# Kernel tuning notes

Hardware: AMD Instinct MI355X
Metric: run time of the kernel (lower is better)

Reference implementation:

```python
import jax, jax.numpy as jnp
import numpy as np

B, S, R = 1, 128, 384          # batch, n_seq (MSA rows), n_res
C_M, C_Z, H, D = 256, 128, 8, 32  # msa channels, pair channels, heads, head dim


def layernorm(x, g, b, eps=1e-5):
    mu = jnp.mean(x, axis=-1, keepdims=True)
    var = jnp.var(x, axis=-1, keepdims=True)
    return (x - mu) * jax.lax.rsqrt(var + eps) * g + b


def setup_inputs() -> dict:
    key = jax.random.key(0)
    ks = jax.random.split(key, 10)
    w = lambda k, shape: jax.random.normal(k, shape, jnp.float32) * 0.02
    return {
        "msa_act": jax.random.normal(ks[0], (B, S, R, C_M), jnp.float32),
        "pair_act": jax.random.normal(ks[1], (B, R, R, C_Z), jnp.float32),
        "msa_mask": jnp.ones((B, S, R), jnp.float32),
        "qn_g": jnp.ones((C_M,), jnp.float32),
        "qn_b": jnp.zeros((C_M,), jnp.float32),
        "pn_g": jnp.ones((C_Z,), jnp.float32),
        "pn_b": jnp.zeros((C_Z,), jnp.float32),
        "w_pair": w(ks[2], (C_Z, H)),           # feat_2d_weights (no bias)
        "wq": w(ks[3], (C_M, H, D)),
        "wk": w(ks[4], (C_M, H, D)),
        "wv": w(ks[5], (C_M, H, D)),
        "wg": w(ks[6], (C_M, H, D)),            # gating linear
        "bg": jnp.ones((H, D), jnp.float32),     # gating bias (AF2 inits to 1)
        "wo": w(ks[7], (H, D, C_M)),             # output projection
        "bo": jnp.zeros((C_M,), jnp.float32),
    }


def reference(msa_act, pair_act, msa_mask, qn_g, qn_b, pn_g, pn_b,
              w_pair, wq, wk, wv, wg, bg, wo, bo):
    # pair bias: LN + Linear(c_z -> H), -> [B, 1, H, R, R]
    z = jnp.einsum('bijc,ch->bhij', layernorm(pair_act, pn_g, pn_b), w_pair)[:, None]
    # mask bias: [B, S, 1, 1, R]
    mask_bias = (1e9 * (msa_mask - 1.0))[:, :, None, None, :]

    m = layernorm(msa_act, qn_g, qn_b)
    q = jnp.einsum('bsrc,chd->bshrd', m, wq) * (D ** -0.5)
    k = jnp.einsum('bsrc,chd->bshrd', m, wk)
    v = jnp.einsum('bsrc,chd->bshrd', m, wv)

    logits = jnp.einsum('bshqd,bshkd->bshqk', q, k) + mask_bias + z  # [B,S,H,R,R]
    a = jax.nn.softmax(logits, axis=-1)
    o = jnp.einsum('bshqk,bshkd->bsqhd', a, v)                       # [B,S,R,H,D]

    g = jax.nn.sigmoid(jnp.einsum('bsrc,chd->bsrhd', m, wg) + bg)
    out = jnp.einsum('bsrhd,hdc->bsrc', o * g, wo) + bo              # [B,S,R,C_M]
    return out
```

## Files before the change

kernel.cpp:

```cpp
#include <hip/hip_runtime.h>
#include <hip/hip_bf16.h>

typedef unsigned int uint;
typedef unsigned short ushortT;
typedef __attribute__((ext_vector_type(8))) short bf16x8;
typedef __attribute__((ext_vector_type(4))) float f32x4;

#define S_ 128
#define R_ 384
#define CM 256
#define CZ 128
#define H_ 8
#define D_ 32
#define SR (S_*R_)
#define RRTOT (R_*R_)
#define SHRD (S_*H_*R_*D_)

__device__ __forceinline__ float bf2f(ushortT u) {
    return __uint_as_float(((uint)u) << 16);
}
__device__ __forceinline__ ushortT f2bf(float f) {
    uint x = __float_as_uint(f);
    x += 0x7FFFu + ((x >> 16) & 1u);
    return (ushortT)(x >> 16);
}
__device__ __forceinline__ uint pack_bf2(float lo, float hi) {
    return (uint)f2bf(lo) | ((uint)f2bf(hi) << 16);
}

__global__ __launch_bounds__(256) void k_prep(
        const float* __restrict__ wq, const float* __restrict__ wk,
        const float* __restrict__ wv, const float* __restrict__ wg,
        const float* __restrict__ wo,
        ushortT* __restrict__ wt, ushortT* __restrict__ wgt,
        ushortT* __restrict__ wot) {
    int id = blockIdx.x * 256 + threadIdx.x;
    int which = id >> 16, r16 = id & 65535;
    int y = r16 & 255, x = r16 >> 8;
    if (which == 0)      wt[(size_t)y*256 + x]       = f2bf(wq[(size_t)x*256 + y] * 0.17677669529663687f);
    else if (which == 1) wt[(size_t)(256+y)*256 + x] = f2bf(wk[(size_t)x*256 + y]);
    else if (which == 2) wt[(size_t)(512+y)*256 + x] = f2bf(wv[(size_t)x*256 + y]);
    else if (which == 3) wgt[(size_t)y*256 + x]      = f2bf(wg[(size_t)x*256 + y]);
    else                 wot[(size_t)y*256 + x]      = f2bf(wo[(size_t)x*256 + y]);
}

__global__ __launch_bounds__(256) void k_pair_bias(
        const float* __restrict__ pair, const float* __restrict__ pn_g,
        const float* __restrict__ pn_b, const float* __restrict__ w_pair,
        ushortT* __restrict__ z) {
    int wave = threadIdx.x >> 6, lane = threadIdx.x & 63;
    int row = blockIdx.x * 4 + wave;
    const float* x = pair + (size_t)row * CZ;
    float2 xv = *(const float2*)&x[lane * 2];
    float s  = xv.x + xv.y;
    float s2 = xv.x*xv.x + xv.y*xv.y;
    #pragma unroll
    for (int off = 32; off; off >>= 1) {
        s  += __shfl_xor(s,  off);
        s2 += __shfl_xor(s2, off);
    }
    float mu  = s * (1.0f / 128.0f);
    float var = s2 * (1.0f / 128.0f) - mu * mu;
    float rstd = rsqrtf(var + 1e-5f);
    float2 gv = *(const float2*)&pn_g[lane * 2];
    float2 bv = *(const float2*)&pn_b[lane * 2];
    float n0 = (xv.x - mu) * rstd * gv.x + bv.x;
    float n1 = (xv.y - mu) * rstd * gv.y + bv.y;
    float4 wa = *(const float4*)&w_pair[lane*16     ];
    float4 wb = *(const float4*)&w_pair[lane*16 +  4];
    float4 wc = *(const float4*)&w_pair[lane*16 +  8];
    float4 wd = *(const float4*)&w_pair[lane*16 + 12];
    float v0_ = n0*wa.x + n1*wc.x, v1_ = n0*wa.y + n1*wc.y;
    float v2_ = n0*wa.z + n1*wc.z, v3_ = n0*wa.w + n1*wc.w;
    float v4_ = n0*wb.x + n1*wd.x, v5_ = n0*wb.y + n1*wd.y;
    float v6_ = n0*wb.z + n1*wd.z, v7_ = n0*wb.w + n1*wd.w;
    float x0 = __shfl_xor(v0_,1), x1 = __shfl_xor(v1_,1), x2 = __shfl_xor(v2_,1), x3 = __shfl_xor(v3_,1);
    float x4 = __shfl_xor(v4_,1), x5 = __shfl_xor(v5_,1), x6 = __shfl_xor(v6_,1), x7 = __shfl_xor(v7_,1);
    bool b0 = (lane & 1) != 0;
    float u0 = b0 ? v4_+x4 : v0_+x0;
    float u1 = b0 ? v5_+x5 : v1_+x1;
    float u2 = b0 ? v6_+x6 : v2_+x2;
    float u3 = b0 ? v7_+x7 : v3_+x3;
    float y0 = __shfl_xor(u0,2), y1 = __shfl_xor(u1,2), y2 = __shfl_xor(u2,2), y3 = __shfl_xor(u3,2);
    bool b1 = (lane & 2) != 0;
    float w0 = b1 ? u2+y2 : u0+y0;
    float w1 = b1 ? u3+y3 : u1+y1;
    float z0 = __shfl_xor(w0,4), z1 = __shfl_xor(w1,4);
    bool b2 = (lane & 4) != 0;
    float val = b2 ? w1+z1 : w0+z0;
    val += __shfl_xor(val, 8);
    val += __shfl_xor(val, 16);
    val += __shfl_xor(val, 32);
    int hmap = 4*(lane & 1) + 2*((lane >> 1) & 1) + ((lane >> 2) & 1);
    if (lane < 8) z[(size_t)hmap * RRTOT + row] = f2bf(val);
}

__device__ __forceinline__ void ln_row_f4(
        const float* __restrict__ src, const float* __restrict__ gam,
        const float* __restrict__ bet, char* msb, int row, int lane) {
    float4 xv = *(const float4*)&src[lane * 4];
    float sm = (xv.x + xv.y) + (xv.z + xv.w);
    float s2 = (xv.x*xv.x + xv.y*xv.y) + (xv.z*xv.z + xv.w*xv.w);
    #pragma unroll
    for (int off = 32; off; off >>= 1) {
        sm += __shfl_xor(sm, off);
        s2 += __shfl_xor(s2, off);
    }
    float mu  = sm * (1.0f / 256.0f);
    float var = s2 * (1.0f / 256.0f) - mu * mu;
    float rstd = rsqrtf(var + 1e-5f);
    float4 gv = *(const float4*)&gam[lane * 4];
    float4 bv = *(const float4*)&bet[lane * 4];
    float n0 = (xv.x - mu) * rstd * gv.x + bv.x, n1 = (xv.y - mu) * rstd * gv.y + bv.y;
    float n2 = (xv.z - mu) * rstd * gv.z + bv.z, n3 = (xv.w - mu) * rstd * gv.w + bv.w;
    uint2 w; w.x = pack_bf2(n0, n1); w.y = pack_bf2(n2, n3);
    *(uint2*)(msb + ((row*512 + lane*8) ^ ((row & 7) << 4))) = w;
}

__global__ __launch_bounds__(256) void k_msa_qkv(
        const float* __restrict__ msa, const float* __restrict__ qn_g,
        const float* __restrict__ qn_b, const ushortT* __restrict__ wt,
        ushortT* __restrict__ qo, ushortT* __restrict__ ko,
        ushortT* __restrict__ vto) {
    __shared__ ushortT m_sh[32 * 256];
    __shared__ ushortT st_sh[3 * 32 * 256];
    int tid = threadIdx.x, wave = tid >> 6, lane = tid & 63;
    int c = lane & 15, g = (lane >> 4) & 3;
    int r0 = blockIdx.x * 32, s = r0 / R_, rl0 = r0 % R_;
    char* msb = (char*)m_sh;
    char* stb = (char*)st_sh;

    #pragma unroll
    for (int i = 0; i < 8; ++i) {
        int row = wave * 8 + i;
        ln_row_f4(msa + (size_t)(r0 + row) * CM, qn_g, qn_b, msb, row, lane);
    }
    __syncthreads();

    bf16x8 af[2][8];
    #pragma unroll
    for (int rt = 0; rt < 2; ++rt)
        #pragma unroll
        for (int kc = 0; kc < 8; ++kc) {
            int row = rt*16 + c;
            af[rt][kc] = *(const bf16x8*)(msb + ((row*512 + (kc*32 + 8*g)*2) ^ ((c & 7) << 4)));
        }

    const f32x4 z4 = {0.f, 0.f, 0.f, 0.f};
    #pragma unroll
    for (int mI = 0; mI < 3; ++mI) {
        char* osb = stb + mI * 16384;
        int tb = wave * 4;
        const ushortT* wb0 = wt + ((size_t)(mI*256 + tb*16 + c)) * 256 + 8*g;
        const ushortT* wb1 = wb0 + 16*256;
        const ushortT* wb2 = wb0 + 32*256;
        const ushortT* wb3 = wb0 + 48*256;
        f32x4 a0L = z4, a0H = z4, a1L = z4, a1H = z4;
        f32x4 a2L = z4, a2H = z4, a3L = z4, a3H = z4;
        #pragma unroll
        for (int kc = 0; kc < 8; ++kc) {
            bf16x8 b0 = *(const bf16x8*)(wb0 + kc*32);
            bf16x8 b1 = *(const bf16x8*)(wb1 + kc*32);
            bf16x8 b2 = *(const bf16x8*)(wb2 + kc*32);
            bf16x8 b3 = *(const bf16x8*)(wb3 + kc*32);
            a0L = __builtin_amdgcn_mfma_f32_16x16x32_bf16(af[0][kc], b0, a0L, 0, 0, 0);
            a0H = __builtin_amdgcn_mfma_f32_16x16x32_bf16(af[1][kc], b0, a0H, 0, 0, 0);
            a1L = __builtin_amdgcn_mfma_f32_16x16x32_bf16(af[0][kc], b1, a1L, 0, 0, 0);
            a1H = __builtin_amdgcn_mfma_f32_16x16x32_bf16(af[1][kc], b1, a1H, 0, 0, 0);
            a2L = __builtin_amdgcn_mfma_f32_16x16x32_bf16(af[0][kc], b2, a2L, 0, 0, 0);
            a2H = __builtin_amdgcn_mfma_f32_16x16x32_bf16(af[1][kc], b2, a2H, 0, 0, 0);
            a3L = __builtin_amdgcn_mfma_f32_16x16x32_bf16(af[0][kc], b3, a3L, 0, 0, 0);
            a3H = __builtin_amdgcn_mfma_f32_16x16x32_bf16(af[1][kc], b3, a3H, 0, 0, 0);
        }
        #pragma unroll
        for (int j = 0; j < 4; ++j) {
            f32x4 lo = (j == 0) ? a0L : (j == 1) ? a1L : (j == 2) ? a2L : a3L;
            f32x4 hi = (j == 0) ? a0H : (j == 1) ? a1H : (j == 2) ? a2H : a3H;
            if (mI < 2) {
                int col = (tb + j)*16 + c;
                #pragma unroll
                for (int r = 0; r < 4; ++r) {
                    int row0 = 4*g + r, row1 = row0 + 16;
                    *(ushortT*)(osb + ((row0*512 + col*2) ^ ((row0 & 7) << 4))) = f2bf(lo[r]);
                    *(ushortT*)(osb + ((row1*512 + col*2) ^ ((row1 & 7) << 4))) = f2bf(hi[r]);
                }
            } else {
                int hd = (tb + j)*16 + c;
                #pragma unroll
                for (int r = 0; r < 4; ++r) {
                    int rlo = 4*g + r, rhi = rlo + 16;
                    *(ushortT*)(osb + ((hd*64 + rlo*2) ^ ((hd & 3) << 4))) = f2bf(lo[r]);
                    *(ushortT*)(osb + ((hd*64 + rhi*2) ^ ((hd & 3) << 4))) = f2bf(hi[r]);
                }
            }
        }
    }
    __syncthreads();

    #pragma unroll
    for (int m = 0; m < 2; ++m) {
        char* osb = stb + m * 16384;
        ushortT* O = (m == 0) ? qo : ko;
        #pragma unroll
        for (int i = 0; i < 4; ++i) {
            int idx = tid + i*256;
            int row = idx >> 5, c16 = idx & 31;
            uint4 vd = *(const uint4*)(osb + ((row*512 + c16*16) ^ ((row & 7) << 4)));
            int hh = c16 >> 2, dq = (c16 & 3) * 8;
            size_t ga = ((size_t)(s*H_ + hh) * R_ + rl0 + row) * D_ + dq;
            *(uint4*)&O[ga] = vd;
        }
    }
    {
        char* osb = stb + 2 * 16384;
        #pragma unroll
        for (int i = 0; i < 4; ++i) {
            int idx = tid + i*256;
            int hd = idx >> 2, q8 = idx & 3;
            uint4 vd = *(const uint4*)(osb + ((hd*64 + q8*16) ^ ((hd & 3) << 4)));
            size_t ga = ((size_t)(s*256 + hd)) * R_ + rl0 + q8*8;
            *(uint4*)&vto[ga] = vd;
        }
    }
}

__global__ __launch_bounds__(512) void k_attn(
        const ushortT* __restrict__ qws, const ushortT* __restrict__ kws,
        const ushortT* __restrict__ vtws, const ushortT* __restrict__ zws,
        const float* __restrict__ mask, float* __restrict__ out) {
    __shared__ ushortT k_sh[R_ * 40];
    __shared__ ushortT vt_sh[D_ * R_];
    __shared__ float   mb[R_];
    __shared__ ushortT p_sh[8 * 1280];
    int tid = threadIdx.x, wave = tid >> 6, lane = tid & 63;
    int c = lane & 15, g = (lane >> 4) & 3;
    int s = blockIdx.x >> 3, h = blockIdx.x & 7;
    size_t base = (size_t)(s * H_ + h) * R_ * D_;

    {
        const uint4* ks = (const uint4*)(kws + base);
        char* kb_ = (char*)k_sh;
        for (int i = tid; i < 1536; i += 512) {
            int row = i >> 2, part = i & 3;
            *(uint4*)(kb_ + row*80 + part*16) = ks[i];
        }
        const uint4* vs = (const uint4*)(vtws + base);
        char* vb = (char*)vt_sh;
        for (int i = tid; i < 1536; i += 512) {
            int d = i / 48, ch = i % 48;
            *(uint4*)(vb + ((d*768 + ch*16) ^ ((d & 7) << 4))) = vs[i];
        }
        for (int j = tid; j < R_; j += 512) mb[j] = 1e9f * (mask[s*R_ + j] - 1.0f);
    }
    __syncthreads();

    const char* ksb = (const char*)k_sh;
    const char* vtb = (const char*)vt_sh;
    char* psb = (char*)p_sh + wave * 2560;
    const f32x4 zero4 = {0.f, 0.f, 0.f, 0.f};

    for (int qt = wave; qt < 24; qt += 8) {
        int q0 = qt * 16;
        bf16x8 qf = *(const bf16x8*)(qws + base + (size_t)(q0 + c) * D_ + 8*g);
        const ushortT* zq = zws + (size_t)h * RRTOT + (size_t)(q0 + c) * R_ + 4*g;

        float sm = 0.f;
        f32x4 o0 = zero4, o1 = zero4;
        #pragma unroll 2
        for (int kb = 0; kb < 12; ++kb) {
            bf16x8 kfA = *(const bf16x8*)(ksb + ((2*kb    )*16 + c)*80 + 16*g);
            bf16x8 kfB = *(const bf16x8*)(ksb + ((2*kb + 1)*16 + c)*80 + 16*g);
            f32x4 pA = __builtin_amdgcn_mfma_f32_16x16x32_bf16(kfA, qf, zero4, 0, 0, 0);
            f32x4 pB = __builtin_amdgcn_mfma_f32_16x16x32_bf16(kfB, qf, zero4, 0, 0, 0);
            float4 mvA = *(const float4*)&mb[(2*kb    )*16 + 4*g];
            float4 mvB = *(const float4*)&mb[(2*kb + 1)*16 + 4*g];
            ushort4 zvA = *(const ushort4*)(zq + (2*kb    )*16);
            ushort4 zvB = *(const ushort4*)(zq + (2*kb + 1)*16);
            pA.x = __expf(pA.x + mvA.x + bf2f(zvA.x));
            pA.y = __expf(pA.y + mvA.y + bf2f(zvA.y));
            pA.z = __expf(pA.z + mvA.z + bf2f(zvA.z));
            pA.w = __expf(pA.w + mvA.w + bf2f(zvA.w));
            pB.x = __expf(pB.x + mvB.x + bf2f(zvB.x));
            pB.y = __expf(pB.y + mvB.y + bf2f(zvB.y));
            pB.z = __expf(pB.z + mvB.z + bf2f(zvB.z));
            pB.w = __expf(pB.w + mvB.w + bf2f(zvB.w));
            sm += (pA.x + pA.y) + (pA.z + pA.w) + (pB.x + pB.y) + (pB.z + pB.w);
            uint2 wA; wA.x = pack_bf2(pA.x, pA.y); wA.y = pack_bf2(pA.z, pA.w);
            uint2 wB; wB.x = pack_bf2(pB.x, pB.y); wB.y = pack_bf2(pB.z, pB.w);
            *(uint2*)(psb + (kb&1)*1280 + c*80 +      8*g) = wA;
            *(uint2*)(psb + (kb&1)*1280 + c*80 + 32 + 8*g) = wB;
            bf16x8 pa = *(const bf16x8*)(psb + (kb&1)*1280 + c*80 + 16*g);
            bf16x8 v0 = *(const bf16x8*)(vtb + (((c     )*768 + kb*64 + 16*g) ^ ((c & 7) << 4)));
            bf16x8 v1 = *(const bf16x8*)(vtb + (((16 + c)*768 + kb*64 + 16*g) ^ ((c & 7) << 4)));
            o0 = __builtin_amdgcn_mfma_f32_16x16x32_bf16(v0, pa, o0, 0, 0, 0);
            o1 = __builtin_amdgcn_mfma_f32_16x16x32_bf16(v1, pa, o1, 0, 0, 0);
        }
        sm += __shfl_xor(sm, 16);
        sm += __shfl_xor(sm, 32);
        float inv = 1.0f / sm;
        float4 s0, s1;
        s0.x = o0[0]*inv; s0.y = o0[1]*inv; s0.z = o0[2]*inv; s0.w = o0[3]*inv;
        s1.x = o1[0]*inv; s1.y = o1[1]*inv; s1.z = o1[2]*inv; s1.w = o1[3]*inv;
        float* ob = out + (size_t)(s*R_ + q0 + c) * CM + h*D_ + 4*g;
        *(float4*)ob = s0;
        *(float4*)(ob + 16) = s1;
    }
}

__global__ __launch_bounds__(256) void k_out(
        const float* __restrict__ msa, const float* __restrict__ qn_g,
        const float* __restrict__ qn_b, const ushortT* __restrict__ wgt,
        const float* __restrict__ bg, const ushortT* __restrict__ wot,
        const float* __restrict__ bo, float* __restrict__ out) {
    __shared__ ushortT m_sh[32 * 256];
    __shared__ ushortT og_sh[32 * 256];
    int tid = threadIdx.x, wave = tid >> 6, lane = tid & 63;
    int c = lane & 15, g = (lane >> 4) & 3;
    int r0 = blockIdx.x * 32;
    char* msb = (char*)m_sh;
    char* ogb = (char*)og_sh;

    #pragma unroll
    for (int i = 0; i < 8; ++i) {
        int row = wave * 8 + i;
        ln_row_f4(msa + (size_t)(r0 + row) * CM, qn_g, qn_b, msb, row, lane);
    }
    __syncthreads();

    bf16x8 af[2][8];
    #pragma unroll
    for (int rt = 0; rt < 2; ++rt)
        #pragma unroll
        for (int kc = 0; kc < 8; ++kc) {
            int row = rt*16 + c;
            af[rt][kc] = *(const bf16x8*)(msb + ((row*512 + (kc*32 + 8*g)*2) ^ ((c & 7) << 4)));
        }

    const f32x4 z4 = {0.f, 0.f, 0.f, 0.f};
    {
        int tb = wave * 4;
        const ushortT* wb0 = wgt + (size_t)(tb*16 + c) * 256 + 8*g;
        const ushortT* wb1 = wb0 + 16*256;
        const ushortT* wb2 = wb0 + 32*256;
        const ushortT* wb3 = wb0 + 48*256;
        f32x4 a0L = z4, a0H = z4, a1L = z4, a1H = z4;
        f32x4 a2L = z4, a2H = z4, a3L = z4, a3H = z4;
        #pragma unroll
        for (int kc = 0; kc < 8; ++kc) {
            bf16x8 b0 = *(const bf16x8*)(wb0 + kc*32);
            bf16x8 b1 = *(const bf16x8*)(wb1 + kc*32);
            bf16x8 b2 = *(const bf16x8*)(wb2 + kc*32);
            bf16x8 b3 = *(const bf16x8*)(wb3 + kc*32);
            a0L = __builtin_amdgcn_mfma_f32_16x16x32_bf16(af[0][kc], b0, a0L, 0, 0, 0);
            a0H = __builtin_amdgcn_mfma_f32_16x16x32_bf16(af[1][kc], b0, a0H, 0, 0, 0);
            a1L = __builtin_amdgcn_mfma_f32_16x16x32_bf16(af[0][kc], b1, a1L, 0, 0, 0);
            a1H = __builtin_amdgcn_mfma_f32_16x16x32_bf16(af[1][kc], b1, a1H, 0, 0, 0);
            a2L = __builtin_amdgcn_mfma_f32_16x16x32_bf16(af[0][kc], b2, a2L, 0, 0, 0);
            a2H = __builtin_amdgcn_mfma_f32_16x16x32_bf16(af[1][kc], b2, a2H, 0, 0, 0);
            a3L = __builtin_amdgcn_mfma_f32_16x16x32_bf16(af[0][kc], b3, a3L, 0, 0, 0);
            a3H = __builtin_amdgcn_mfma_f32_16x16x32_bf16(af[1][kc], b3, a3H, 0, 0, 0);
        }
        #pragma unroll
        for (int j = 0; j < 4; ++j) {
            f32x4 lo = (j == 0) ? a0L : (j == 1) ? a1L : (j == 2) ? a2L : a3L;
            f32x4 hi = (j == 0) ? a0H : (j == 1) ? a1H : (j == 2) ? a2H : a3H;
            int t = (tb + j)*16 + c;
            float bgv = bg[t];
            #pragma unroll
            for (int r = 0; r < 4; ++r) {
                int row0 = 4*g + r, row1 = row0 + 16;
                float g0 = 1.0f / (1.0f + __expf(-(lo[r] + bgv)));
                float g1 = 1.0f / (1.0f + __expf(-(hi[r] + bgv)));
                float ov0 = out[(size_t)(r0 + row0) * CM + t];
                float ov1 = out[(size_t)(r0 + row1) * CM + t];
                *(ushortT*)(ogb + ((row0*512 + t*2) ^ ((row0 & 7) << 4))) = f2bf(ov0 * g0);
                *(ushortT*)(ogb + ((row1*512 + t*2) ^ ((row1 & 7) << 4))) = f2bf(ov1 * g1);
            }
        }
    }
    __syncthreads();

    bf16x8 af2[2][8];
    #pragma unroll
    for (int rt = 0; rt < 2; ++rt)
        #pragma unroll
        for (int kc = 0; kc < 8; ++kc) {
            int row = rt*16 + c;
            af2[rt][kc] = *(const bf16x8*)(ogb + ((row*512 + (kc*32 + 8*g)*2) ^ ((c & 7) << 4)));
        }

    {
        int tb = wave * 4;
        const ushortT* wb0 = wot + (size_t)(tb*16 + c) * 256 + 8*g;
        const ushortT* wb1 = wb0 + 16*256;
        const ushortT* wb2 = wb0 + 32*256;
        const ushortT* wb3 = wb0 + 48*256;
        f32x4 a0L = z4, a0H = z4, a1L = z4, a1H = z4;
        f32x4 a2L = z4, a2H = z4, a3L = z4, a3H = z4;
        #pragma unroll
        for (int kc = 0; kc < 8; ++kc) {
            bf16x8 b0 = *(const bf16x8*)(wb0 + kc*32);
            bf16x8 b1 = *(const bf16x8*)(wb1 + kc*32);
            bf16x8 b2 = *(const bf16x8*)(wb2 + kc*32);
            bf16x8 b3 = *(const bf16x8*)(wb3 + kc*32);
            a0L = __builtin_amdgcn_mfma_f32_16x16x32_bf16(af2[0][kc], b0, a0L, 0, 0, 0);
            a0H = __builtin_amdgcn_mfma_f32_16x16x32_bf16(af2[1][kc], b0, a0H, 0, 0, 0);
            a1L = __builtin_amdgcn_mfma_f32_16x16x32_bf16(af2[0][kc], b1, a1L, 0, 0, 0);
            a1H = __builtin_amdgcn_mfma_f32_16x16x32_bf16(af2[1][kc], b1, a1H, 0, 0, 0);
            a2L = __builtin_amdgcn_mfma_f32_16x16x32_bf16(af2[0][kc], b2, a2L, 0, 0, 0);
            a2H = __builtin_amdgcn_mfma_f32_16x16x32_bf16(af2[1][kc], b2, a2H, 0, 0, 0);
            a3L = __builtin_amdgcn_mfma_f32_16x16x32_bf16(af2[0][kc], b3, a3L, 0, 0, 0);
            a3H = __builtin_amdgcn_mfma_f32_16x16x32_bf16(af2[1][kc], b3, a3H, 0, 0, 0);
        }
        #pragma unroll
        for (int j = 0; j < 4; ++j) {
            f32x4 lo = (j == 0) ? a0L : (j == 1) ? a1L : (j == 2) ? a2L : a3L;
            f32x4 hi = (j == 0) ? a0H : (j == 1) ? a1H : (j == 2) ? a2H : a3H;
            int t = (tb + j)*16 + c;
            float bov = bo[t];
            #pragma unroll
            for (int r = 0; r < 4; ++r) {
                int row0 = 4*g + r, row1 = row0 + 16;
                out[(size_t)(r0 + row0) * CM + t] = lo[r] + bov;
                out[(size_t)(r0 + row1) * CM + t] = hi[r] + bov;
            }
        }
    }
}

extern "C" void kernel_launch(void* const* d_in, const int* in_sizes, int n_in,
                              void* d_out, int out_size, void* d_ws, size_t ws_size,
                              hipStream_t stream) {
    const float* msa    = (const float*)d_in[0];
    const float* pair   = (const float*)d_in[1];
    const float* mask   = (const float*)d_in[2];
    const float* qn_g   = (const float*)d_in[3];
    const float* qn_b   = (const float*)d_in[4];
    const float* pn_g   = (const float*)d_in[5];
    const float* pn_b   = (const float*)d_in[6];
    const float* w_pair = (const float*)d_in[7];
    const float* wq     = (const float*)d_in[8];
    const float* wk     = (const float*)d_in[9];
    const float* wv     = (const float*)d_in[10];
    const float* wg     = (const float*)d_in[11];
    const float* bg     = (const float*)d_in[12];
    const float* wo     = (const float*)d_in[13];
    const float* bo     = (const float*)d_in[14];
    float* out = (float*)d_out;

    ushortT* qws  = (ushortT*)d_ws;
    ushortT* kws  = qws + (size_t)SHRD;
    ushortT* vtws = kws + (size_t)SHRD;
    ushortT* zws  = vtws + (size_t)SHRD;
    ushortT* wt   = zws + (size_t)H_ * RRTOT;
    ushortT* wgt  = wt + 3 * 65536;
    ushortT* wot  = wgt + 65536;

    k_prep     <<<1280,    256, 0, stream>>>(wq, wk, wv, wg, wo, wt, wgt, wot);
    k_pair_bias<<<RRTOT/4, 256, 0, stream>>>(pair, pn_g, pn_b, w_pair, zws);
    k_msa_qkv  <<<SR/32,   256, 0, stream>>>(msa, qn_g, qn_b, wt, qws, kws, vtws);
    k_attn     <<<S_*H_,   512, 0, stream>>>(qws, kws, vtws, zws, mask, out);
    k_out      <<<SR/32,   256, 0, stream>>>(msa, qn_g, qn_b, wgt, bg, wot, bo, out);
}
```

Measured before the change: 273.8 us.

## Split MSA layernorm into its own kernel and reuse bf16 result in projections

```diff
diff --git a/kernel.cpp b/kernel.cpp
--- a/kernel.cpp
+++ b/kernel.cpp
@@ -95,29 +95,231 @@
     if (lane < 8) z[(size_t)hmap * RRTOT + row] = f2bf(val);
 }
 
+__device__ __forceinline__ uint2 ln_reduce(float4 xv, float4 gv, float4 bv) {
+    float sm = (xv.x + xv.y) + (xv.z + xv.w);
+    float s2 = (xv.x*xv.x + xv.y*xv.y) + (xv.z*xv.z + xv.w*xv.w);
+    #pragma unroll
+    for (int off = 32; off; off >>= 1) {
+        sm += __shfl_xor(sm, off);
+        s2 += __shfl_xor(s2, off);
+    }
+    float mu  = sm * (1.0f / 256.0f);
+    float var = s2 * (1.0f / 256.0f) - mu * mu;
+    float rstd = rsqrtf(var + 1e-5f);
+    uint2 w;
+    w.x = pack_bf2((xv.x - mu)*rstd*gv.x + bv.x, (xv.y - mu)*rstd*gv.y + bv.y);
+    w.y = pack_bf2((xv.z - mu)*rstd*gv.z + bv.z, (xv.w - mu)*rstd*gv.w + bv.w);
+    return w;
+}
+
+__global__ __launch_bounds__(256) void k_ln(
+        const float* __restrict__ msa, const float* __restrict__ qn_g,
+        const float* __restrict__ qn_b, ushortT* __restrict__ m) {
+    int wave = threadIdx.x >> 6, lane = threadIdx.x & 63;
+    int r0 = blockIdx.x * 32 + wave * 8;
+    const float* src = msa + (size_t)r0 * CM + lane * 4;
+    float4 x0 = *(const float4*)(src         );
+    float4 x1 = *(const float4*)(src + 1*CM  );
+    float4 x2 = *(const float4*)(src + 2*CM  );
+    float4 x3 = *(const float4*)(src + 3*CM  );
+    float4 x4 = *(const float4*)(src + 4*CM  );
+    float4 x5 = *(const float4*)(src + 5*CM  );
+    float4 x6 = *(const float4*)(src + 6*CM  );
+    float4 x7 = *(const float4*)(src + 7*CM  );
+    float4 gv = *(const float4*)&qn_g[lane*4];
+    float4 bv = *(const float4*)&qn_b[lane*4];
+    ushortT* dst = m + (size_t)r0 * CM + lane * 4;
+    *(uint2*)(dst        ) = ln_reduce(x0, gv, bv);
+    *(uint2*)(dst + 1*CM ) = ln_reduce(x1, gv, bv);
+    *(uint2*)(dst + 2*CM ) = ln_reduce(x2, gv, bv);
+    *(uint2*)(dst + 3*CM ) = ln_reduce(x3, gv, bv);
+    *(uint2*)(dst + 4*CM ) = ln_reduce(x4, gv, bv);
+    *(uint2*)(dst + 5*CM ) = ln_reduce(x5, gv, bv);
+    *(uint2*)(dst + 6*CM ) = ln_reduce(x6, gv, bv);
+    *(uint2*)(dst + 7*CM ) = ln_reduce(x7, gv, bv);
+}
+
+#define MFMA_GROUP4(AF, WB)                                                          \
+    {                                                                                \
+        _Pragma("unroll")                                                            \
+        for (int kc = 0; kc < 8; ++kc) {                                             \
+            bf16x8 b0 = *(const bf16x8*)((WB) + kc*32);                              \
+            bf16x8 b1 = *(const bf16x8*)((WB) + 16*256 + kc*32);                     \
+            bf16x8 b2 = *(const bf16x8*)((WB) + 32*256 + kc*32);                     \
+            bf16x8 b3 = *(const bf16x8*)((WB) + 48*256 + kc*32);                     \
+            a0L = __builtin_amdgcn_mfma_f32_16x16x32_bf16(AF[0][kc], b0, a0L, 0,0,0);\
+            a0H = __builtin_amdgcn_mfma_f32_16x16x32_bf16(AF[1][kc], b0, a0H, 0,0,0);\
+            a1L = __builtin_amdgcn_mfma_f32_16x16x32_bf16(AF[0][kc], b1, a1L, 0,0,0);\
+            a1H = __builtin_amdgcn_mfma_f32_16x16x32_bf16(AF[1][kc], b1, a1H, 0,0,0);\
+            a2L = __builtin_amdgcn_mfma_f32_16x16x32_bf16(AF[0][kc], b2, a2L, 0,0,0);\
+            a2H = __builtin_amdgcn_mfma_f32_16x16x32_bf16(AF[1][kc], b2, a2H, 0,0,0);\
+            a3L = __builtin_amdgcn_mfma_f32_16x16x32_bf16(AF[0][kc], b3, a3L, 0,0,0);\
+            a3H = __builtin_amdgcn_mfma_f32_16x16x32_bf16(AF[1][kc], b3, a3H, 0,0,0);\
+        }                                                                            \
+    }
+
+__global__ __launch_bounds__(256) void k_qkv(
+        const ushortT* __restrict__ m, const ushortT* __restrict__ wt,
+        ushortT* __restrict__ qo, ushortT* __restrict__ ko,
+        ushortT* __restrict__ vto) {
+    __shared__ ushortT st_sh[4 * 32 * 256];
+    int tid = threadIdx.x, wave = tid >> 6, lane = tid & 63;
+    int c = lane & 15, g = (lane >> 4) & 3;
+    int r0 = blockIdx.x * 128, wrow = wave * 32;
+    int s = r0 / R_, rl0 = r0 % R_ + wrow;
+    char* osb = (char*)st_sh + wave * 16384;
+
+    bf16x8 af[2][8];
+    #pragma unroll
+    for (int rt = 0; rt < 2; ++rt)
+        #pragma unroll
+        for (int kc = 0; kc < 8; ++kc)
+            af[rt][kc] = *(const bf16x8*)(m + (size_t)(r0 + wrow + rt*16 + c) * CM + kc*32 + 8*g);
+
+    const f32x4 z4 = {0.f, 0.f, 0.f, 0.f};
+    #pragma unroll
+    for (int mI = 0; mI < 3; ++mI) {
+        #pragma unroll
+        for (int grp = 0; grp < 4; ++grp) {
+            int tb = grp * 4;
+            const ushortT* wb0 = wt + ((size_t)(mI*256 + tb*16 + c)) * 256 + 8*g;
+            f32x4 a0L = z4, a0H = z4, a1L = z4, a1H = z4;
+            f32x4 a2L = z4, a2H = z4, a3L = z4, a3H = z4;
+            MFMA_GROUP4(af, wb0);
+            #pragma unroll
+            for (int j = 0; j < 4; ++j) {
+                f32x4 lo = (j == 0) ? a0L : (j == 1) ? a1L : (j == 2) ? a2L : a3L;
+                f32x4 hi = (j == 0) ? a0H : (j == 1) ? a1H : (j == 2) ? a2H : a3H;
+                if (mI < 2) {
+                    int col = (tb + j)*16 + c;
+                    #pragma unroll
+                    for (int r = 0; r < 4; ++r) {
+                        int row0 = 4*g + r, row1 = row0 + 16;
+                        *(ushortT*)(osb + ((row0*512 + col*2) ^ ((row0 & 7) << 4))) = f2bf(lo[r]);
+                        *(ushortT*)(osb + ((row1*512 + col*2) ^ ((row1 & 7) << 4))) = f2bf(hi[r]);
+                    }
+                } else {
+                    int hd = (tb + j)*16 + c;
+                    #pragma unroll
+                    for (int r = 0; r < 4; ++r) {
+                        int rlo = 4*g + r, rhi = rlo + 16;
+                        *(ushortT*)(osb + ((hd*64 + rlo*2) ^ ((hd & 3) << 4))) = f2bf(lo[r]);
+                        *(ushortT*)(osb + ((hd*64 + rhi*2) ^ ((hd & 3) << 4))) = f2bf(hi[r]);
+                    }
+                }
+            }
+        }
+        if (mI < 2) {
+            ushortT* O = (mI == 0) ? qo : ko;
+            #pragma unroll
+            for (int i = 0; i < 16; ++i) {
+                int chunk = lane + i*64;
+                int row = chunk >> 5, c16 = chunk & 31;
+                uint4 vd = *(const uint4*)(osb + ((row*512 + c16*16) ^ ((row & 7) << 4)));
+                int hh = c16 >> 2, dq = (c16 & 3) * 8;
+                size_t ga = ((size_t)(s*H_ + hh) * R_ + rl0 + row) * D_ + dq;
+                *(uint4*)&O[ga] = vd;
+            }
+        } else {
+            #pragma unroll
+            for (int i = 0; i < 16; ++i) {
+                int chunk = lane + i*64;
+                int hd = chunk >> 2, q8 = chunk & 3;
+                uint4 vd = *(const uint4*)(osb + ((hd*64 + q8*16) ^ ((hd & 3) << 4)));
+                size_t ga = ((size_t)(s*256 + hd)) * R_ + rl0 + q8*8;
+                *(uint4*)&vto[ga] = vd;
+            }
+        }
+    }
+}
+
+__global__ __launch_bounds__(256) void k_out_m(
+        const ushortT* __restrict__ m, const ushortT* __restrict__ wgt,
+        const float* __restrict__ bg, const ushortT* __restrict__ wot,
+        const float* __restrict__ bo, float* __restrict__ out) {
+    __shared__ ushortT og_sh[4 * 32 * 256];
+    int tid = threadIdx.x, wave = tid >> 6, lane = tid & 63;
+    int c = lane & 15, g = (lane >> 4) & 3;
+    int r0 = blockIdx.x * 128, wrow = wave * 32;
+    char* ogb = (char*)og_sh + wave * 16384;
+
+    bf16x8 af[2][8];
+    #pragma unroll
+    for (int rt = 0; rt < 2; ++rt)
+        #pragma unroll
+        for (int kc = 0; kc < 8; ++kc)
+            af[rt][kc] = *(const bf16x8*)(m + (size_t)(r0 + wrow + rt*16 + c) * CM + kc*32 + 8*g);
+
+    const f32x4 z4 = {0.f, 0.f, 0.f, 0.f};
+    #pragma unroll
+    for (int grp = 0; grp < 4; ++grp) {
+        int tb = grp * 4;
+        const ushortT* wb0 = wgt + (size_t)(tb*16 + c) * 256 + 8*g;
+        f32x4 a0L = z4, a0H = z4, a1L = z4, a1H = z4;
+        f32x4 a2L = z4, a2H = z4, a3L = z4, a3H = z4;
+        MFMA_GROUP4(af, wb0);
+        #pragma unroll
+        for (int j = 0; j < 4; ++j) {
+            f32x4 lo = (j == 0) ? a0L : (j == 1) ? a1L : (j == 2) ? a2L : a3L;
+            f32x4 hi = (j == 0) ? a0H : (j == 1) ? a1H : (j == 2) ? a2H : a3H;
+            int t = (tb + j)*16 + c;
+            float bgv = bg[t];
+            #pragma unroll
+            for (int r = 0; r < 4; ++r) {
+                int row0 = 4*g + r, row1 = row0 + 16;
+                float g0 = 1.0f / (1.0f + __expf(-(lo[r] + bgv)));
+                float g1 = 1.0f / (1.0f + __expf(-(hi[r] + bgv)));
+                float ov0 = out[(size_t)(r0 + wrow + row0) * CM + t];
+                float ov1 = out[(size_t)(r0 + wrow + row1) * CM + t];
+                *(ushortT*)(ogb + ((row0*512 + t*2) ^ ((row0 & 7) << 4))) = f2bf(ov0 * g0);
+                *(ushortT*)(ogb + ((row1*512 + t*2) ^ ((row1 & 7) << 4))) = f2bf(ov1 * g1);
+            }
+        }
+    }
+
+    bf16x8 af2[2][8];
+    #pragma unroll
+    for (int rt = 0; rt < 2; ++rt)
+        #pragma unroll
+        for (int kc = 0; kc < 8; ++kc) {
+            int row = rt*16 + c;
+            af2[rt][kc] = *(const bf16x8*)(ogb + ((row*512 + (kc*32 + 8*g)*2) ^ ((c & 7) << 4)));
+        }
+
+    #pragma unroll
+    for (int grp = 0; grp < 4; ++grp) {
+        int tb = grp * 4;
+        const ushortT* wb0 = wot + (size_t)(tb*16 + c) * 256 + 8*g;
+        f32x4 a0L = z4, a0H = z4, a1L = z4, a1H = z4;
+        f32x4 a2L = z4, a2H = z4, a3L = z4, a3H = z4;
+        MFMA_GROUP4(af2, wb0);
+        #pragma unroll
+        for (int j = 0; j < 4; ++j) {
+            f32x4 lo = (j == 0) ? a0L : (j == 1) ? a1L : (j == 2) ? a2L : a3L;
+            f32x4 hi = (j == 0) ? a0H : (j == 1) ? a1H : (j == 2) ? a2H : a3H;
+            int t = (tb + j)*16 + c;
+            float bov = bo[t];
+            #pragma unroll
+            for (int r = 0; r < 4; ++r) {
+                int row0 = 4*g + r, row1 = row0 + 16;
+                out[(size_t)(r0 + wrow + row0) * CM + t] = lo[r] + bov;
+                out[(size_t)(r0 + wrow + row1) * CM + t] = hi[r] + bov;
+            }
+        }
+    }
+}
+
 __device__ __forceinline__ void ln_row_f4(
         const float* __restrict__ src, const float* __restrict__ gam,
         const float* __restrict__ bet, char* msb, int row, int lane) {
     float4 xv = *(const float4*)&src[lane * 4];
-    float sm = (xv.x + xv.y) + (xv.z + xv.w);
-    float s2 = (xv.x*xv.x + xv.y*xv.y) + (xv.z*xv.z + xv.w*xv.w);
-    #pragma unroll
-    for (int off = 32; off; off >>= 1) {
-        sm += __shfl_xor(sm, off);
-        s2 += __shfl_xor(s2, off);
-    }
-    float mu  = sm * (1.0f / 256.0f);
-    float var = s2 * (1.0f / 256.0f) - mu * mu;
-    float rstd = rsqrtf(var + 1e-5f);
     float4 gv = *(const float4*)&gam[lane * 4];
     float4 bv = *(const float4*)&bet[lane * 4];
-    float n0 = (xv.x - mu) * rstd * gv.x + bv.x, n1 = (xv.y - mu) * rstd * gv.y + bv.y;
-    float n2 = (xv.z - mu) * rstd * gv.z + bv.z, n3 = (xv.w - mu) * rstd * gv.w + bv.w;
-    uint2 w; w.x = pack_bf2(n0, n1); w.y = pack_bf2(n2, n3);
+    uint2 w = ln_reduce(xv, gv, bv);
     *(uint2*)(msb + ((row*512 + lane*8) ^ ((row & 7) << 4))) = w;
 }
 
-__global__ __launch_bounds__(256) void k_msa_qkv(
+__global__ __launch_bounds__(256) void k_msa_qkv_fb(
         const float* __restrict__ msa, const float* __restrict__ qn_g,
         const float* __restrict__ qn_b, const ushortT* __restrict__ wt,
         ushortT* __restrict__ qo, ushortT* __restrict__ ko,
@@ -129,14 +331,10 @@
     int r0 = blockIdx.x * 32, s = r0 / R_, rl0 = r0 % R_;
     char* msb = (char*)m_sh;
     char* stb = (char*)st_sh;
-
-    #pragma unroll
-    for (int i = 0; i < 8; ++i) {
-        int row = wave * 8 + i;
-        ln_row_f4(msa + (size_t)(r0 + row) * CM, qn_g, qn_b, msb, row, lane);
-    }
+    #pragma unroll
+    for (int i = 0; i < 8; ++i)
+        ln_row_f4(msa + (size_t)(r0 + wave*8 + i) * CM, qn_g, qn_b, msb, wave*8 + i, lane);
     __syncthreads();
-
     bf16x8 af[2][8];
     #pragma unroll
     for (int rt = 0; rt < 2; ++rt)
@@ -145,33 +343,15 @@
             int row = rt*16 + c;
             af[rt][kc] = *(const bf16x8*)(msb + ((row*512 + (kc*32 + 8*g)*2) ^ ((c & 7) << 4)));
         }
-
     const f32x4 z4 = {0.f, 0.f, 0.f, 0.f};
     #pragma unroll
     for (int mI = 0; mI < 3; ++mI) {
         char* osb = stb + mI * 16384;
         int tb = wave * 4;
         const ushortT* wb0 = wt + ((size_t)(mI*256 + tb*16 + c)) * 256 + 8*g;
-        const ushortT* wb1 = wb0 + 16*256;
-        const ushortT* wb2 = wb0 + 32*256;
-        const ushortT* wb3 = wb0 + 48*256;
         f32x4 a0L = z4, a0H = z4, a1L = z4, a1H = z4;
         f32x4 a2L = z4, a2H = z4, a3L = z4, a3H = z4;
-        #pragma unroll
-        for (int kc = 0; kc < 8; ++kc) {
-            bf16x8 b0 = *(const bf16x8*)(wb0 + kc*32);
-            bf16x8 b1 = *(const bf16x8*)(wb1 + kc*32);
-            bf16x8 b2 = *(const bf16x8*)(wb2 + kc*32);
-            bf16x8 b3 = *(const bf16x8*)(wb3 + kc*32);
-            a0L = __builtin_amdgcn_mfma_f32_16x16x32_bf16(af[0][kc], b0, a0L, 0, 0, 0);
-            a0H = __builtin_amdgcn_mfma_f32_16x16x32_bf16(af[1][kc], b0, a0H, 0, 0, 0);
-            a1L = __builtin_amdgcn_mfma_f32_16x16x32_bf16(af[0][kc], b1, a1L, 0, 0, 0);
-            a1H = __builtin_amdgcn_mfma_f32_16x16x32_bf16(af[1][kc], b1, a1H, 0, 0, 0);
-            a2L = __builtin_amdgcn_mfma_f32_16x16x32_bf16(af[0][kc], b2, a2L, 0, 0, 0);
-            a2H = __builtin_amdgcn_mfma_f32_16x16x32_bf16(af[1][kc], b2, a2H, 0, 0, 0);
-            a3L = __builtin_amdgcn_mfma_f32_16x16x32_bf16(af[0][kc], b3, a3L, 0, 0, 0);
-            a3H = __builtin_amdgcn_mfma_f32_16x16x32_bf16(af[1][kc], b3, a3H, 0, 0, 0);
-        }
+        MFMA_GROUP4(af, wb0);
         #pragma unroll
         for (int j = 0; j < 4; ++j) {
             f32x4 lo = (j == 0) ? a0L : (j == 1) ? a1L : (j == 2) ? a2L : a3L;
@@ -196,11 +376,10 @@
         }
     }
     __syncthreads();
-
-    #pragma unroll
-    for (int m = 0; m < 2; ++m) {
-        char* osb = stb + m * 16384;
-        ushortT* O = (m == 0) ? qo : ko;
+    #pragma unroll
+    for (int mm = 0; mm < 2; ++mm) {
+        char* osb = stb + mm * 16384;
+        ushortT* O = (mm == 0) ? qo : ko;
         #pragma unroll
         for (int i = 0; i < 4; ++i) {
             int idx = tid + i*256;
@@ -220,6 +399,86 @@
             uint4 vd = *(const uint4*)(osb + ((hd*64 + q8*16) ^ ((hd & 3) << 4)));
             size_t ga = ((size_t)(s*256 + hd)) * R_ + rl0 + q8*8;
             *(uint4*)&vto[ga] = vd;
+        }
+    }
+}
+
+__global__ __launch_bounds__(256) void k_out_fb(
+        const float* __restrict__ msa, const float* __restrict__ qn_g,
+        const float* __restrict__ qn_b, const ushortT* __restrict__ wgt,
+        const float* __restrict__ bg, const ushortT* __restrict__ wot,
+        const float* __restrict__ bo, float* __restrict__ out) {
+    __shared__ ushortT m_sh[32 * 256];
+    __shared__ ushortT og_sh[32 * 256];
+    int tid = threadIdx.x, wave = tid >> 6, lane = tid & 63;
+    int c = lane & 15, g = (lane >> 4) & 3;
+    int r0 = blockIdx.x * 32;
+    char* msb = (char*)m_sh;
+    char* ogb = (char*)og_sh;
+    #pragma unroll
+    for (int i = 0; i < 8; ++i)
+        ln_row_f4(msa + (size_t)(r0 + wave*8 + i) * CM, qn_g, qn_b, msb, wave*8 + i, lane);
+    __syncthreads();
+    bf16x8 af[2][8];
+    #pragma unroll
+    for (int rt = 0; rt < 2; ++rt)
+        #pragma unroll
+        for (int kc = 0; kc < 8; ++kc) {
+            int row = rt*16 + c;
+            af[rt][kc] = *(const bf16x8*)(msb + ((row*512 + (kc*32 + 8*g)*2) ^ ((c & 7) << 4)));
+        }
+    const f32x4 z4 = {0.f, 0.f, 0.f, 0.f};
+    {
+        int tb = wave * 4;
+        const ushortT* wb0 = wgt + (size_t)(tb*16 + c) * 256 + 8*g;
+        f32x4 a0L = z4, a0H = z4, a1L = z4, a1H = z4;
+        f32x4 a2L = z4, a2H = z4, a3L = z4, a3H = z4;
+        MFMA_GROUP4(af, wb0);
+        #pragma unroll
+        for (int j = 0; j < 4; ++j) {
+            f32x4 lo = (j == 0) ? a0L : (j == 1) ? a1L : (j == 2) ? a2L : a3L;
+            f32x4 hi = (j == 0) ? a0H : (j == 1) ? a1H : (j == 2) ? a2H : a3H;
+            int t = (tb + j)*16 + c;
+            float bgv = bg[t];
+            #pragma unroll
+            for (int r = 0; r < 4; ++r) {
+                int row0 = 4*g + r, row1 = row0 + 16;
+                float g0 = 1.0f / (1.0f + __expf(-(lo[r] + bgv)));
+                float g1 = 1.0f / (1.0f + __expf(-(hi[r] + bgv)));
+                float ov0 = out[(size_t)(r0 + row0) * CM + t];
+                float ov1 = out[(size_t)(r0 + row1) * CM + t];
+                *(ushortT*)(ogb + ((row0*512 + t*2) ^ ((row0 & 7) << 4))) = f2bf(ov0 * g0);
+                *(ushortT*)(ogb + ((row1*512 + t*2) ^ ((row1 & 7) << 4))) = f2bf(ov1 * g1);
+            }
+        }
+    }
+    __syncthreads();
+    bf16x8 af2[2][8];
+    #pragma unroll
+    for (int rt = 0; rt < 2; ++rt)
+        #pragma unroll
+        for (int kc = 0; kc < 8; ++kc) {
+            int row = rt*16 + c;
+            af2[rt][kc] = *(const bf16x8*)(ogb + ((row*512 + (kc*32 + 8*g)*2) ^ ((c & 7) << 4)));
+        }
+    {
+        int tb = wave * 4;
+        const ushortT* wb0 = wot + (size_t)(tb*16 + c) * 256 + 8*g;
+        f32x4 a0L = z4, a0H = z4, a1L = z4, a1H = z4;
+        f32x4 a2L = z4, a2H = z4, a3L = z4, a3H = z4;
+        MFMA_GROUP4(af2, wb0);
+        #pragma unroll
+        for (int j = 0; j < 4; ++j) {
+            f32x4 lo = (j == 0) ? a0L : (j == 1) ? a1L : (j == 2) ? a2L : a3L;
+            f32x4 hi = (j == 0) ? a0H : (j == 1) ? a1H : (j == 2) ? a2H : a3H;
+            int t = (tb + j)*16 + c;
+            float bov = bo[t];
+            #pragma unroll
+            for (int r = 0; r < 4; ++r) {
+                int row0 = 4*g + r, row1 = row0 + 16;
+                out[(size_t)(r0 + row0) * CM + t] = lo[r] + bov;
+                out[(size_t)(r0 + row1) * CM + t] = hi[r] + bov;
+            }
         }
     }
 }
@@ -307,127 +566,6 @@
     }
 }
 
-__global__ __launch_bounds__(256) void k_out(
-        const float* __restrict__ msa, const float* __restrict__ qn_g,
-        const float* __restrict__ qn_b, const ushortT* __restrict__ wgt,
-        const float* __restrict__ bg, const ushortT* __restrict__ wot,
-        const float* __restrict__ bo, float* __restrict__ out) {
-    __shared__ ushortT m_sh[32 * 256];
-    __shared__ ushortT og_sh[32 * 256];
-    int tid = threadIdx.x, wave = tid >> 6, lane = tid & 63;
-    int c = lane & 15, g = (lane >> 4) & 3;
-    int r0 = blockIdx.x * 32;
-    char* msb = (char*)m_sh;
-    char* ogb = (char*)og_sh;
-
-    #pragma unroll
-    for (int i = 0; i < 8; ++i) {
-        int row = wave * 8 + i;
-        ln_row_f4(msa + (size_t)(r0 + row) * CM, qn_g, qn_b, msb, row, lane);
-    }
-    __syncthreads();
-
-    bf16x8 af[2][8];
-    #pragma unroll
-    for (int rt = 0; rt < 2; ++rt)
-        #pragma unroll
-        for (int kc = 0; kc < 8; ++kc) {
-            int row = rt*16 + c;
-            af[rt][kc] = *(const bf16x8*)(msb + ((row*512 + (kc*32 + 8*g)*2) ^ ((c & 7) << 4)));
-        }
-
-    const f32x4 z4 = {0.f, 0.f, 0.f, 0.f};
-    {
-        int tb = wave * 4;
-        const ushortT* wb0 = wgt + (size_t)(tb*16 + c) * 256 + 8*g;
-        const ushortT* wb1 = wb0 + 16*256;
-        const ushortT* wb2 = wb0 + 32*256;
-        const ushortT* wb3 = wb0 + 48*256;
-        f32x4 a0L = z4, a0H = z4, a1L = z4, a1H = z4;
-        f32x4 a2L = z4, a2H = z4, a3L = z4, a3H = z4;
-        #pragma unroll
-        for (int kc = 0; kc < 8; ++kc) {
-            bf16x8 b0 = *(const bf16x8*)(wb0 + kc*32);
-            bf16x8 b1 = *(const bf16x8*)(wb1 + kc*32);
-            bf16x8 b2 = *(const bf16x8*)(wb2 + kc*32);
-            bf16x8 b3 = *(const bf16x8*)(wb3 + kc*32);
-            a0L = __builtin_amdgcn_mfma_f32_16x16x32_bf16(af[0][kc], b0, a0L, 0, 0, 0);
-            a0H = __builtin_amdgcn_mfma_f32_16x16x32_bf16(af[1][kc], b0, a0H, 0, 0, 0);
-            a1L = __builtin_amdgcn_mfma_f32_16x16x32_bf16(af[0][kc], b1, a1L, 0, 0, 0);
-            a1H = __builtin_amdgcn_mfma_f32_16x16x32_bf16(af[1][kc], b1, a1H, 0, 0, 0);
-            a2L = __builtin_amdgcn_mfma_f32_16x16x32_bf16(af[0][kc], b2, a2L, 0, 0, 0);
-            a2H = __builtin_amdgcn_mfma_f32_16x16x32_bf16(af[1][kc], b2, a2H, 0, 0, 0);
-            a3L = __builtin_amdgcn_mfma_f32_16x16x32_bf16(af[0][kc], b3, a3L, 0, 0, 0);
-            a3H = __builtin_amdgcn_mfma_f32_16x16x32_bf16(af[1][kc], b3, a3H, 0, 0, 0);
-        }
-        #pragma unroll
-        for (int j = 0; j < 4; ++j) {
-            f32x4 lo = (j == 0) ? a0L : (j == 1) ? a1L : (j == 2) ? a2L : a3L;
-            f32x4 hi = (j == 0) ? a0H : (j == 1) ? a1H : (j == 2) ? a2H : a3H;
-            int t = (tb + j)*16 + c;
-            float bgv = bg[t];
-            #pragma unroll
-            for (int r = 0; r < 4; ++r) {
-                int row0 = 4*g + r, row1 = row0 + 16;
-                float g0 = 1.0f / (1.0f + __expf(-(lo[r] + bgv)));
-                float g1 = 1.0f / (1.0f + __expf(-(hi[r] + bgv)));
-                float ov0 = out[(size_t)(r0 + row0) * CM + t];
-                float ov1 = out[(size_t)(r0 + row1) * CM + t];
-                *(ushortT*)(ogb + ((row0*512 + t*2) ^ ((row0 & 7) << 4))) = f2bf(ov0 * g0);
-                *(ushortT*)(ogb + ((row1*512 + t*2) ^ ((row1 & 7) << 4))) = f2bf(ov1 * g1);
-            }
-        }
-    }
-    __syncthreads();
-
-    bf16x8 af2[2][8];
-    #pragma unroll
-    for (int rt = 0; rt < 2; ++rt)
-        #pragma unroll
-        for (int kc = 0; kc < 8; ++kc) {
-            int row = rt*16 + c;
-            af2[rt][kc] = *(const bf16x8*)(ogb + ((row*512 + (kc*32 + 8*g)*2) ^ ((c & 7) << 4)));
-        }
-
-    {
-        int tb = wave * 4;
-        const ushortT* wb0 = wot + (size_t)(tb*16 + c) * 256 + 8*g;
-        const ushortT* wb1 = wb0 + 16*256;
-        const ushortT* wb2 = wb0 + 32*256;
-        const ushortT* wb3 = wb0 + 48*256;
-        f32x4 a0L = z4, a0H = z4, a1L = z4, a1H = z4;
-        f32x4 a2L = z4, a2H = z4, a3L = z4, a3H = z4;
-        #pragma unroll
-        for (int kc = 0; kc < 8; ++kc) {
-            bf16x8 b0 = *(const bf16x8*)(wb0 + kc*32);
-            bf16x8 b1 = *(const bf16x8*)(wb1 + kc*32);
-            bf16x8 b2 = *(const bf16x8*)(wb2 + kc*32);
-            bf16x8 b3 = *(const bf16x8*)(wb3 + kc*32);
-            a0L = __builtin_amdgcn_mfma_f32_16x16x32_bf16(af2[0][kc], b0, a0L, 0, 0, 0);
-            a0H = __builtin_amdgcn_mfma_f32_16x16x32_bf16(af2[1][kc], b0, a0H, 0, 0, 0);
-            a1L = __builtin_amdgcn_mfma_f32_16x16x32_bf16(af2[0][kc], b1, a1L, 0, 0, 0);
-            a1H = __builtin_amdgcn_mfma_f32_16x16x32_bf16(af2[1][kc], b1, a1H, 0, 0, 0);
-            a2L = __builtin_amdgcn_mfma_f32_16x16x32_bf16(af2[0][kc], b2, a2L, 0, 0, 0);
-            a2H = __builtin_amdgcn_mfma_f32_16x16x32_bf16(af2[1][kc], b2, a2H, 0, 0, 0);
-            a3L = __builtin_amdgcn_mfma_f32_16x16x32_bf16(af2[0][kc], b3, a3L, 0, 0, 0);
-            a3H = __builtin_amdgcn_mfma_f32_16x16x32_bf16(af2[1][kc], b3, a3H, 0, 0, 0);
-        }
-        #pragma unroll
-        for (int j = 0; j < 4; ++j) {
-            f32x4 lo = (j == 0) ? a0L : (j == 1) ? a1L : (j == 2) ? a2L : a3L;
-            f32x4 hi = (j == 0) ? a0H : (j == 1) ? a1H : (j == 2) ? a2H : a3H;
-            int t = (tb + j)*16 + c;
-            float bov = bo[t];
-            #pragma unroll
-            for (int r = 0; r < 4; ++r) {
-                int row0 = 4*g + r, row1 = row0 + 16;
-                out[(size_t)(r0 + row0) * CM + t] = lo[r] + bov;
-                out[(size_t)(r0 + row1) * CM + t] = hi[r] + bov;
-            }
-        }
-    }
-}
-
 extern "C" void kernel_launch(void* const* d_in, const int* in_sizes, int n_in,
                               void* d_out, int out_size, void* d_ws, size_t ws_size,
                               hipStream_t stream) {
@@ -455,10 +593,20 @@
     ushortT* wt   = zws + (size_t)H_ * RRTOT;
     ushortT* wgt  = wt + 3 * 65536;
     ushortT* wot  = wgt + 65536;
+    ushortT* mws  = wot + 65536;
+
+    size_t need = ((size_t)3*SHRD + (size_t)H_*RRTOT + 5*65536 + (size_t)SR*CM) * 2;
 
     k_prep     <<<1280,    256, 0, stream>>>(wq, wk, wv, wg, wo, wt, wgt, wot);
     k_pair_bias<<<RRTOT/4, 256, 0, stream>>>(pair, pn_g, pn_b, w_pair, zws);
-    k_msa_qkv  <<<SR/32,   256, 0, stream>>>(msa, qn_g, qn_b, wt, qws, kws, vtws);
-    k_attn     <<<S_*H_,   512, 0, stream>>>(qws, kws, vtws, zws, mask, out);
-    k_out      <<<SR/32,   256, 0, stream>>>(msa, qn_g, qn_b, wgt, bg, wot, bo, out);
-}
+    if (ws_size >= need) {
+        k_ln   <<<SR/32,   256, 0, stream>>>(msa, qn_g, qn_b, mws);
+        k_qkv  <<<SR/128,  256, 0, stream>>>(mws, wt, qws, kws, vtws);
+        k_attn <<<S_*H_,   512, 0, stream>>>(qws, kws, vtws, zws, mask, out);
+        k_out_m<<<SR/128,  256, 0, stream>>>(mws, wgt, bg, wot, bo, out);
+    } else {
+        k_msa_qkv_fb<<<SR/32, 256, 0, stream>>>(msa, qn_g, qn_b, wt, qws, kws, vtws);
+        k_attn      <<<S_*H_, 512, 0, stream>>>(qws, kws, vtws, zws, mask, out);
+        k_out_fb    <<<SR/32, 256, 0, stream>>>(msa, qn_g, qn_b, wgt, bg, wot, bo, out);
+    }
+}
```

Result: slower. 340.0 us (+24.2%).
